# Optimization experiments

Hardware: AMD Instinct MI355X
Metric: run time of the kernel (lower is better)

## Reference

```python
import jax, jax.numpy as jnp
import numpy as np

PATCH = 14

def _patchify(t, p):
    # (B,C,H,W) -> (B*pH*pW, C, p*p)
    B, C, H, W = t.shape
    pH, pW = H // p, W // p
    t = t.reshape(B, C, pH, p, pW, p).transpose(0, 2, 4, 1, 3, 5)
    return t.reshape(B * pH * pW, C, p * p)

def _unpatchify(t, B, C, H, W, p):
    pH, pW = H // p, W // p
    t = t.reshape(B, pH, pW, C, p, p).transpose(0, 3, 1, 4, 2, 5)
    return t.reshape(B, C, H, W)

def setup_inputs() -> dict:
    key = jax.random.key(0)
    ks = jax.random.split(key, 9)
    B, C, H, W = 4, 256, 224, 224
    s = 1.0 / np.sqrt(C)
    return {
        "x": jax.random.normal(ks[0], (B, C, H, W), jnp.float32),
        "skip0": jax.random.normal(ks[1], (B, C, 112, 112), jnp.float32),
        "skip1": jax.random.normal(ks[2], (B, C, 56, 56), jnp.float32),
        "Wq": jax.random.normal(ks[3], (C, C), jnp.float32) * s,
        "bq": jax.random.normal(ks[4], (C,), jnp.float32) * 0.01,
        "Wk": jax.random.normal(ks[5], (C, C), jnp.float32) * s,
        "bk": jax.random.normal(ks[6], (C,), jnp.float32) * 0.01,
        "Wv": jax.random.normal(ks[7], (C, C), jnp.float32) * s,
        "bv": jax.random.normal(ks[8], (C,), jnp.float32) * 0.01,
    }

def reference(x, skip0, skip1, Wq, bq, Wk, bk, Wv, bv):
    B, C, H, W = x.shape
    p = PATCH
    xp = _patchify(x, p)                       # (N, C, L), L = p*p
    # 1x1 conv on x (query) is shared across skips
    Q = jnp.einsum('oc,ncl->nol', Wq, xp) + bq[None, :, None]
    out = 0.0
    for skip in (skip0, skip1):
        sk = jax.image.resize(skip, (B, C, H, W), method='bilinear')  # align_corners=False
        sp = _patchify(sk, p)
        K = jnp.einsum('oc,ncl->nol', Wk, sp) + bk[None, :, None]
        V = jnp.einsum('oc,ncl->nol', Wv, sp) + bv[None, :, None]
        attn = jax.nn.softmax(jnp.einsum('ncl,ncm->nlm', Q, K), axis=-1)  # unscaled, per original
        out = out + jnp.einsum('nlm,ncm->ncl', attn, V)
    return _unpatchify(out, B, C, H, W, p)
```

## Files before the change

### kernel.cpp

```cpp
#include <hip/hip_runtime.h>

typedef _Float16 f16;
typedef _Float16 f16x8 __attribute__((ext_vector_type(8)));
typedef float f32x4 __attribute__((ext_vector_type(4)));

#define DEV static __device__ __forceinline__

constexpr int  NPATCH = 1024;
constexpr int  LLEN   = 196;
constexpr long NLROWS = (long)NPATCH * LLEN;

DEV void g2l16(const void* g, void* l) {
  __builtin_amdgcn_global_load_lds(
      (const __attribute__((address_space(1))) unsigned int*)g,
      (__attribute__((address_space(3))) unsigned int*)l, 16, 0, 0);
}

DEV unsigned pk2(float a, float b) {
  union { f16 h[2]; unsigned u; } z;
  z.h[0] = (f16)a; z.h[1] = (f16)b;
  return z.u;
}

__global__ __launch_bounds__(256) void k0_prep(
    const float* __restrict__ Wq, const float* __restrict__ Wk,
    const float* __restrict__ Wv, const float* __restrict__ bq,
    f16* __restrict__ G16, f16* __restrict__ Wv16, float* __restrict__ u32) {
  int bx = blockIdx.x, t = threadIdx.x;
  if (bx < 256) {
    int c = bx;
    float acc = 0.f;
    for (int o = 0; o < 256; ++o) acc += Wq[o*256 + c] * Wk[o*256 + t];
    G16[c*256 + t] = (f16)acc;
  } else if (bx == 256) {
    float acc = 0.f;
    for (int o = 0; o < 256; ++o) acc += bq[o] * Wk[o*256 + t];
    u32[t] = acc;
  } else {
    for (int r = 0; r < 256; ++r) Wv16[r*256 + t] = (f16)Wv[r*256 + t];
  }
}

__global__ __launch_bounds__(256) void k1_pack(
    const float* __restrict__ src, int Hs, int Ws, float invS,
    f16* __restrict__ dst, float* __restrict__ ub4,
    const float* __restrict__ u32, int do_ub) {
  __shared__ unsigned tile[32 * 225];
  __shared__ float us[64];
  int bx = blockIdx.x;
  int cc0 = (bx & 3) * 64;
  int bi = bx >> 2;
  int i  = bi % 14; bi /= 14;
  int py = bi & 15; int b = bi >> 4;
  int y = py*14 + i;
  int t = threadIdx.x;
  if (t < 64) us[t] = u32[cc0 + t];

  if (invS == 1.0f) {
    int xh = t & 7, pr = t >> 3;
    const float* b0 = src + ((long)(b*256 + cc0 + 2*pr)) * 50176 + y*224;
    const float* b1 = b0 + 50176;
#pragma unroll
    for (int it = 0; it < 7; ++it) {
      int x0 = (it*8 + xh) * 4;
      float4 va = *(const float4*)(b0 + x0);
      float4 vb = *(const float4*)(b1 + x0);
      tile[pr*225 + x0 + 0] = pk2(va.x, vb.x);
      tile[pr*225 + x0 + 1] = pk2(va.y, vb.y);
      tile[pr*225 + x0 + 2] = pk2(va.z, vb.z);
      tile[pr*225 + x0 + 3] = pk2(va.w, vb.w);
    }
  } else {
    float fy  = (y + 0.5f) * invS - 0.5f;
    float y0f = floorf(fy);
    float wy1 = fy - y0f, wy0 = 1.f - wy1;
    int y0 = (int)y0f, y1 = (int)y0f + 1;
    y0 = min(max(y0, 0), Hs-1); y1 = min(max(y1, 0), Hs-1);
    long plane = (long)Hs * Ws;
    int xl = t & 63, c4 = t >> 6;
    for (int xp = 0; xp < 4; ++xp) {
      int x = xp*64 + xl;
      if (x < 224) {
        float fx  = (x + 0.5f) * invS - 0.5f;
        float x0f = floorf(fx);
        float wx1 = fx - x0f, wx0 = 1.f - wx1;
        int x0 = (int)x0f, x1 = (int)x0f + 1;
        x0 = min(max(x0, 0), Ws-1); x1 = min(max(x1, 0), Ws-1);
        int o00 = y0*Ws + x0, o01 = y0*Ws + x1;
        int o10 = y1*Ws + x0, o11 = y1*Ws + x1;
#pragma unroll
        for (int pp = 0; pp < 8; ++pp) {
          int pr = c4*8 + pp;
          const float* base0 = src + ((long)(b*256 + cc0 + 2*pr)) * plane;
          const float* base1 = base0 + plane;
          float va = wy0*(wx0*base0[o00] + wx1*base0[o01])
                   + wy1*(wx0*base0[o10] + wx1*base0[o11]);
          float vb = wy0*(wx0*base1[o00] + wx1*base1[o01])
                   + wy1*(wx0*base1[o10] + wx1*base1[o11]);
          tile[pr*225 + x] = pk2(va, vb);
        }
      }
    }
  }
  __syncthreads();
  int q = t & 7, xg = t >> 3;
  float4 u0, u1;
  if (do_ub) {
    u0 = *(const float4*)(us + q*8);
    u1 = *(const float4*)(us + q*8 + 4);
  }
  for (int xo = 0; xo < 7; ++xo) {
    int x = xo*32 + xg;
    unsigned p0 = tile[(q*4+0)*225 + x];
    unsigned p1 = tile[(q*4+1)*225 + x];
    unsigned p2 = tile[(q*4+2)*225 + x];
    unsigned p3 = tile[(q*4+3)*225 + x];
    int px = x / 14, j = x % 14;
    int m = i*14 + j;
    long nm = (long)(b*256 + py*16 + px) * 196 + m;
    uint4 w; w.x = p0; w.y = p1; w.z = p2; w.w = p3;
    *reinterpret_cast<uint4*>(dst + nm*256 + cc0 + q*8) = w;
    if (do_ub) {
      union { unsigned u; f16 h[2]; } c0, c1, c2, c3;
      c0.u = p0; c1.u = p1; c2.u = p2; c3.u = p3;
      float part = u0.x*(float)c0.h[0] + u0.y*(float)c0.h[1]
                 + u0.z*(float)c1.h[0] + u0.w*(float)c1.h[1]
                 + u1.x*(float)c2.h[0] + u1.y*(float)c2.h[1]
                 + u1.z*(float)c3.h[0] + u1.w*(float)c3.h[1];
      part += __shfl_xor(part, 1);
      part += __shfl_xor(part, 2);
      part += __shfl_xor(part, 4);
      if (q == 0) ub4[(long)(bx & 3) * NLROWS + nm] = part;
    }
  }
}

__global__ __launch_bounds__(256) void k2_kv(
    const f16* __restrict__ SPT, const f16* __restrict__ G16,
    const f16* __restrict__ Wv16, f16* __restrict__ KtT, f16* __restrict__ VT2) {
  __shared__ __align__(16) char ldsA[64 * 80];
  __shared__ __align__(16) char ldsB[512 * 80];
  int tid = threadIdx.x;
  int lane = tid & 63, wv = tid >> 6;
  long nm0 = (long)blockIdx.x * 64;
  f32x4 zero = {0.f, 0.f, 0.f, 0.f};
  f32x4 acc[4][8];
#pragma unroll
  for (int a = 0; a < 4; ++a)
#pragma unroll
    for (int bb = 0; bb < 8; ++bb) acc[a][bb] = zero;
  int col0 = wv * 128;
  int r15 = lane & 15, quad = lane >> 4;
  for (int k0 = 0; k0 < 256; k0 += 32) {
    __syncthreads();
#pragma unroll
    for (int call = 0; call < 2; ++call) {
      int slot = call*256 + tid;
      if (slot < 320) {
        int row = slot / 5, part = slot % 5;
        int pp_ = part < 4 ? part : 0;
        g2l16(SPT + ((nm0 + row)*256 + k0 + pp_*8), ldsA + slot*16);
      }
    }
#pragma unroll
    for (int call = 0; call < 10; ++call) {
      int slot = call*256 + tid;
      int row = slot / 5, part = slot % 5;
      int pp_ = part < 4 ? part : 0;
      const f16* g = (row < 256) ? (G16 + (row*256 + k0 + pp_*8))
                                 : (Wv16 + ((row - 256)*256 + k0 + pp_*8));
      g2l16(g, ldsB + slot*16);
    }
    __syncthreads();
    f16x8 af[4];
#pragma unroll
    for (int rt = 0; rt < 4; ++rt)
      af[rt] = *(const f16x8*)(ldsA + (rt*16 + r15)*80 + quad*16);
#pragma unroll
    for (int tc = 0; tc < 8; ++tc) {
      f16x8 bf = *(const f16x8*)(ldsB + (col0 + tc*16 + r15)*80 + quad*16);
#pragma unroll
      for (int rt = 0; rt < 4; ++rt)
        acc[rt][tc] = __builtin_amdgcn_mfma_f32_16x16x32_f16(af[rt], bf, acc[rt][tc], 0, 0, 0);
    }
  }
  __syncthreads();
  f16* ldsV = (f16*)ldsB;
  if (wv >= 2) {
#pragma unroll
    for (int rt = 0; rt < 4; ++rt)
#pragma unroll
      for (int tc = 0; tc < 8; ++tc) {
        int o = col0 - 256 + tc*16 + r15;
#pragma unroll
        for (int reg = 0; reg < 4; ++reg) {
          int row = rt*16 + quad*4 + reg;
          ldsV[row*258 + o] = (f16)acc[rt][tc][reg];
        }
      }
  } else {
#pragma unroll
    for (int rt = 0; rt < 4; ++rt)
#pragma unroll
      for (int tc = 0; tc < 8; ++tc) {
        int colc = col0 + tc*16 + r15;
#pragma unroll
        for (int reg = 0; reg < 4; ++reg) {
          long row = nm0 + rt*16 + quad*4 + reg;
          KtT[row*256 + colc] = (f16)acc[rt][tc][reg];
        }
      }
  }
  __syncthreads();
  {
    int row = tid & 63;
    long nm = nm0 + row;
    int n = (int)(nm / 196), m = (int)(nm % 196);
    long vbase = ((long)n * 256) * 224 + m;
    int o0 = (tid >> 6) * 64;
    for (int it = 0; it < 64; ++it) {
      int o = o0 + it;
      VT2[vbase + (long)o * 224] = ldsV[row*258 + o];
    }
  }
}

__global__ __launch_bounds__(256) void k3_sv(
    const f16* __restrict__ XT, const f16* __restrict__ KtT,
    const float* __restrict__ ub, const f16* __restrict__ VT2,
    f16* __restrict__ Obuf, int mode) {
  __shared__ __align__(16) char lds[50176];
  __shared__ float ubs[208];
  char* ldsA = lds;
  char* ldsB = lds + 5120;
  char* ldsV = lds + 29696;
  int tid = threadIdx.x;
  int lane = tid & 63, wv = tid >> 6;
  int bx = blockIdx.x;
  int n  = ((bx >> 5) << 3) | (bx & 7);
  int l0 = ((bx >> 3) & 3) * 64;
  long base = (long)n * 196;
  for (int s = tid; s < 208; s += 256) {
    float v = 0.f;
    if (s < 196) {
      long o = base + s;
      v = ub[o] + ub[NLROWS + o] + ub[2*NLROWS + o] + ub[3*NLROWS + o];
    }
    ubs[s] = v;
  }
  f32x4 zero = {0.f, 0.f, 0.f, 0.f};
  f32x4 acc[13];
#pragma unroll
  for (int t = 0; t < 13; ++t) acc[t] = zero;
  int r15 = lane & 15, quad = lane >> 4;
  long vrow = ((long)(n*256)) * 224;

  for (int k0 = 0; k0 < 256; k0 += 32) {
    __syncthreads();
#pragma unroll
    for (int call = 0; call < 2; ++call) {
      int slot = call*256 + tid;
      if (slot < 320) {
        int row = slot / 5, part = slot % 5;
        int pp_ = part < 4 ? part : 0;
        int l = l0 + row; l = l > 195 ? 195 : l;
        g2l16(XT + ((base + l)*256 + k0 + pp_*8), ldsA + slot*16);
      }
    }
#pragma unroll
    for (int call = 0; call < 5; ++call) {
      int slot = call*256 + tid;
      if (slot < 1040) {
        int row = slot / 5, part = slot % 5;
        int pp_ = part < 8 ? (part < 4 ? part : 0) : 0;
        int m = row > 195 ? 195 : row;
        g2l16(KtT + ((base + m)*256 + k0 + pp_*8), ldsB + slot*16);
      }
    }
    __syncthreads();
    f16x8 af = *(const f16x8*)(ldsA + (wv*16 + r15)*80 + quad*16);
#pragma unroll
    for (int t = 0; t < 13; ++t) {
      f16x8 bf = *(const f16x8*)(ldsB + (t*16 + r15)*80 + quad*16);
      acc[t] = __builtin_amdgcn_mfma_f32_16x16x32_f16(af, bf, acc[t], 0, 0, 0);
    }
  }

#pragma unroll
  for (int call = 0; call < 5; ++call) {
    int slot = call*256 + tid;
    int row = slot / 5, part = slot % 5;
    int pp_ = part < 4 ? part : 0;
    g2l16(VT2 + (vrow + (long)row*224 + pp_*8), ldsV + slot*16);
  }

  float mx[4] = {-1e30f, -1e30f, -1e30f, -1e30f};
#pragma unroll
  for (int t = 0; t < 13; ++t) {
    int colb = t*16 + r15;
    float ubv = ubs[colb];
    bool valid = colb < 196;
#pragma unroll
    for (int reg = 0; reg < 4; ++reg) {
      float v = acc[t][reg] + ubv;
      acc[t][reg] = v;
      if (valid) mx[reg] = fmaxf(mx[reg], v);
    }
  }
#pragma unroll
  for (int reg = 0; reg < 4; ++reg) {
    float m = mx[reg];
    m = fmaxf(m, __shfl_xor(m, 1));
    m = fmaxf(m, __shfl_xor(m, 2));
    m = fmaxf(m, __shfl_xor(m, 4));
    m = fmaxf(m, __shfl_xor(m, 8));
    mx[reg] = m;
  }
  float sum[4] = {0.f, 0.f, 0.f, 0.f};
#pragma unroll
  for (int t = 0; t < 13; ++t) {
    int colb = t*16 + r15;
    bool valid = colb < 196;
#pragma unroll
    for (int reg = 0; reg < 4; ++reg) {
      float p = valid ? __expf(acc[t][reg] - mx[reg]) : 0.f;
      acc[t][reg] = p;
      sum[reg] += p;
    }
  }
#pragma unroll
  for (int reg = 0; reg < 4; ++reg) {
    float s = sum[reg];
    s += __shfl_xor(s, 1);
    s += __shfl_xor(s, 2);
    s += __shfl_xor(s, 4);
    s += __shfl_xor(s, 8);
    sum[reg] = 1.0f / s;
  }

  __syncthreads();
#pragma unroll
  for (int reg = 0; reg < 4; ++reg) {
    int row = wv*16 + quad*4 + reg;
    float sc = sum[reg];
#pragma unroll
    for (int t = 0; t < 13; ++t)
      *(f16*)(lds + row*464 + (t*16 + r15)*2) = (f16)(acc[t][reg] * sc);
  }
  {
    int row = tid >> 2, mq = tid & 3;
    *(long*)(lds + row*464 + 416 + mq*8) = 0;
  }

  f32x4 oacc[16];
#pragma unroll
  for (int t = 0; t < 16; ++t) oacc[t] = zero;
  for (int it = 0; it < 7; ++it) {
    if (it > 0) {
      __syncthreads();
#pragma unroll
      for (int call = 0; call < 5; ++call) {
        int slot = call*256 + tid;
        int row = slot / 5, part = slot % 5;
        int pp_ = part < 4 ? part : 0;
        g2l16(VT2 + (vrow + (long)row*224 + it*32 + pp_*8), ldsV + slot*16);
      }
    }
    __syncthreads();
    f16x8 af = *(const f16x8*)(lds + (wv*16 + r15)*464 + it*64 + quad*16);
#pragma unroll
    for (int t = 0; t < 16; ++t) {
      f16x8 bf = *(const f16x8*)(ldsV + (t*16 + r15)*80 + quad*16);
      oacc[t] = __builtin_amdgcn_mfma_f32_16x16x32_f16(af, bf, oacc[t], 0, 0, 0);
    }
  }

#pragma unroll
  for (int reg = 0; reg < 4; ++reg) {
    int l = l0 + wv*16 + quad*4 + reg;
    if (l < 196) {
      long orow = (base + l) * 256;
#pragma unroll
      for (int t = 0; t < 16; ++t) {
        int c = t*16 + r15;
        float v = oacc[t][reg];
        if (mode == 0) Obuf[orow + c] = (f16)v;
        else           Obuf[orow + c] = (f16)(v + (float)Obuf[orow + c]);
      }
    }
  }
}

__global__ __launch_bounds__(256) void k5_unpatch(
    const f16* __restrict__ Obuf, const float* __restrict__ bv,
    float* __restrict__ out) {
  __shared__ float lds[64 * 225];
  int bx = blockIdx.x;
  int cc = (bx & 3) * 64;  bx >>= 2;
  int i  = bx % 14; bx /= 14;
  int py = bx & 15; int b = bx >> 4;
  int t = threadIdx.x;
  int cl = t & 63, pg = t >> 6;
  for (int it = 0; it < 56; ++it) {
    int pr = it*4 + pg;
    int px = pr / 14, j = pr % 14;
    int n = b*256 + py*16 + px;
    float v = (float)Obuf[((long)n*196 + i*14 + j)*256 + cc + cl];
    lds[cl*225 + px*14 + j] = v;
  }
  __syncthreads();
  int yy = py*14 + i;
  for (int c = 0; c < 64; ++c) {
    float bb = 2.0f * bv[cc + c];
    if (t < 224)
      out[(((long)(b*256 + cc + c))*224 + yy)*224 + t] = lds[c*225 + t] + bb;
  }
}

extern "C" void kernel_launch(void* const* d_in, const int* in_sizes, int n_in,
                              void* d_out, int out_size, void* d_ws, size_t ws_size,
                              hipStream_t stream) {
  (void)in_sizes; (void)n_in; (void)out_size; (void)ws_size;
  const float* x     = (const float*)d_in[0];
  const float* skip0 = (const float*)d_in[1];
  const float* skip1 = (const float*)d_in[2];
  const float* Wq    = (const float*)d_in[3];
  const float* bq    = (const float*)d_in[4];
  const float* Wk    = (const float*)d_in[5];
  const float* Wv    = (const float*)d_in[7];
  const float* bv    = (const float*)d_in[8];
  float* out = (float*)d_out;

  char* ws = (char*)d_ws;
  size_t off = 0;
  auto alloc = [&](size_t bytes) {
    char* p = ws + off;
    off += (bytes + 255) & ~(size_t)255;
    return p;
  };
  f16*   XT   = (f16*)  alloc((size_t)NLROWS * 256 * 2);
  f16*   SPT  = (f16*)  alloc((size_t)NLROWS * 256 * 2);
  f16*   KtT  = (f16*)  alloc((size_t)NLROWS * 256 * 2);
  f16*   VT2  = (f16*)  alloc((size_t)NPATCH * 256 * 224 * 2);
  f16*   Obuf = (f16*)  alloc((size_t)NLROWS * 256 * 2);
  float* ub   = (float*)alloc((size_t)NLROWS * 4 * 4);
  f16*   G16  = (f16*)  alloc(256 * 256 * 2);
  f16*   Wv16 = (f16*)  alloc(256 * 256 * 2);
  float* u32  = (float*)alloc(256 * 4);

  k0_prep<<<258, 256, 0, stream>>>(Wq, Wk, Wv, bq, G16, Wv16, u32);
  k1_pack<<<3584, 256, 0, stream>>>(x, 224, 224, 1.0f, XT, nullptr, u32, 0);

  const float* skips[2] = {skip0, skip1};
  int   hs[2]   = {112, 56};
  float invs[2] = {0.5f, 0.25f};
  for (int s = 0; s < 2; ++s) {
    k1_pack<<<3584, 256, 0, stream>>>(skips[s], hs[s], hs[s], invs[s], SPT, ub, u32, 1);
    k2_kv<<<3136, 256, 0, stream>>>(SPT, G16, Wv16, KtT, VT2);
    k3_sv<<<4096, 256, 0, stream>>>(XT, KtT, ub, VT2, Obuf, s);
  }
  k5_unpatch<<<3584, 256, 0, stream>>>(Obuf, bv, out);
}
```

Baseline: 1.556 ms.

## Load K and V operands directly from global memory in the attention kernel

Restructures k3_sv so the 64x256 query tile is staged once into an XOR-swizzled LDS buffer and kept in registers. The K^T and V operands are now read straight from global memory into MFMA registers instead of being staged through LDS with per-step barriers. LDS use shrinks and most __syncthreads disappear, which should raise occupancy and cut synchronisation. The cost is that each wave issues redundant global loads for K and V, relying on L1/L2 to absorb them, and the register count rises.

```diff
diff --git a/kernel.cpp b/kernel.cpp
--- a/kernel.cpp
+++ b/kernel.cpp
@@ -229,17 +229,16 @@
     const f16* __restrict__ XT, const f16* __restrict__ KtT,
     const float* __restrict__ ub, const f16* __restrict__ VT2,
     f16* __restrict__ Obuf, int mode) {
-  __shared__ __align__(16) char lds[50176];
+  __shared__ __align__(16) char lds[64 * 512];
   __shared__ float ubs[208];
-  char* ldsA = lds;
-  char* ldsB = lds + 5120;
-  char* ldsV = lds + 29696;
   int tid = threadIdx.x;
   int lane = tid & 63, wv = tid >> 6;
   int bx = blockIdx.x;
   int n  = ((bx >> 5) << 3) | (bx & 7);
   int l0 = ((bx >> 3) & 3) * 64;
   long base = (long)n * 196;
+  int r15 = lane & 15, quad = lane >> 4;
+
   for (int s = tid; s < 208; s += 256) {
     float v = 0.f;
     if (s < 196) {
@@ -248,50 +247,36 @@
     }
     ubs[s] = v;
   }
+
+#pragma unroll
+  for (int call = 0; call < 8; ++call) {
+    int slot = call*256 + tid;
+    int row = slot >> 5, sc = slot & 31;
+    int l = l0 + row; l = l > 195 ? 195 : l;
+    int gc = sc ^ (row & 7);
+    g2l16(XT + ((base + l)*256 + gc*8), lds + slot*16);
+  }
+  __syncthreads();
+
+  int arow = wv*16 + r15;
+  f16x8 af[8];
+#pragma unroll
+  for (int ks = 0; ks < 8; ++ks)
+    af[ks] = *(const f16x8*)(lds + arow*512 + (((ks*4 + quad) ^ (arow & 7)) * 16));
+
   f32x4 zero = {0.f, 0.f, 0.f, 0.f};
   f32x4 acc[13];
 #pragma unroll
   for (int t = 0; t < 13; ++t) acc[t] = zero;
-  int r15 = lane & 15, quad = lane >> 4;
-  long vrow = ((long)(n*256)) * 224;
-
-  for (int k0 = 0; k0 < 256; k0 += 32) {
-    __syncthreads();
-#pragma unroll
-    for (int call = 0; call < 2; ++call) {
-      int slot = call*256 + tid;
-      if (slot < 320) {
-        int row = slot / 5, part = slot % 5;
-        int pp_ = part < 4 ? part : 0;
-        int l = l0 + row; l = l > 195 ? 195 : l;
-        g2l16(XT + ((base + l)*256 + k0 + pp_*8), ldsA + slot*16);
-      }
-    }
-#pragma unroll
-    for (int call = 0; call < 5; ++call) {
-      int slot = call*256 + tid;
-      if (slot < 1040) {
-        int row = slot / 5, part = slot % 5;
-        int pp_ = part < 8 ? (part < 4 ? part : 0) : 0;
-        int m = row > 195 ? 195 : row;
-        g2l16(KtT + ((base + m)*256 + k0 + pp_*8), ldsB + slot*16);
-      }
-    }
-    __syncthreads();
-    f16x8 af = *(const f16x8*)(ldsA + (wv*16 + r15)*80 + quad*16);
-#pragma unroll
-    for (int t = 0; t < 13; ++t) {
-      f16x8 bf = *(const f16x8*)(ldsB + (t*16 + r15)*80 + quad*16);
-      acc[t] = __builtin_amdgcn_mfma_f32_16x16x32_f16(af, bf, acc[t], 0, 0, 0);
-    }
-  }
-
-#pragma unroll
-  for (int call = 0; call < 5; ++call) {
-    int slot = call*256 + tid;
-    int row = slot / 5, part = slot % 5;
-    int pp_ = part < 4 ? part : 0;
-    g2l16(VT2 + (vrow + (long)row*224 + pp_*8), ldsV + slot*16);
+#pragma unroll
+  for (int t = 0; t < 13; ++t) {
+    int m = t*16 + r15; m = m > 195 ? 195 : m;
+    const f16* kp = KtT + (base + m)*256 + quad*8;
+#pragma unroll
+    for (int ks = 0; ks < 8; ++ks) {
+      f16x8 bf = *(const f16x8*)(kp + ks*32);
+      acc[t] = __builtin_amdgcn_mfma_f32_16x16x32_f16(af[ks], bf, acc[t], 0, 0, 0);
+    }
   }
 
   float mx[4] = {-1e30f, -1e30f, -1e30f, -1e30f};
@@ -351,39 +336,30 @@
     int row = tid >> 2, mq = tid & 3;
     *(long*)(lds + row*464 + 416 + mq*8) = 0;
   }
-
-  f32x4 oacc[16];
-#pragma unroll
-  for (int t = 0; t < 16; ++t) oacc[t] = zero;
-  for (int it = 0; it < 7; ++it) {
-    if (it > 0) {
-      __syncthreads();
-#pragma unroll
-      for (int call = 0; call < 5; ++call) {
-        int slot = call*256 + tid;
-        int row = slot / 5, part = slot % 5;
-        int pp_ = part < 4 ? part : 0;
-        g2l16(VT2 + (vrow + (long)row*224 + it*32 + pp_*8), ldsV + slot*16);
-      }
-    }
-    __syncthreads();
-    f16x8 af = *(const f16x8*)(lds + (wv*16 + r15)*464 + it*64 + quad*16);
-#pragma unroll
-    for (int t = 0; t < 16; ++t) {
-      f16x8 bf = *(const f16x8*)(ldsV + (t*16 + r15)*80 + quad*16);
-      oacc[t] = __builtin_amdgcn_mfma_f32_16x16x32_f16(af, bf, oacc[t], 0, 0, 0);
-    }
-  }
-
-#pragma unroll
-  for (int reg = 0; reg < 4; ++reg) {
-    int l = l0 + wv*16 + quad*4 + reg;
-    if (l < 196) {
-      long orow = (base + l) * 256;
-#pragma unroll
-      for (int t = 0; t < 16; ++t) {
-        int c = t*16 + r15;
-        float v = oacc[t][reg];
+  __syncthreads();
+
+  f16x8 pa[7];
+#pragma unroll
+  for (int it = 0; it < 7; ++it)
+    pa[it] = *(const f16x8*)(lds + (wv*16 + r15)*464 + it*64 + quad*16);
+
+  long vrow = ((long)(n*256)) * 224;
+#pragma unroll
+  for (int t = 0; t < 16; ++t) {
+    const f16* vpt = VT2 + vrow + (long)(t*16 + r15)*224 + quad*8;
+    f32x4 o = zero;
+#pragma unroll
+    for (int it = 0; it < 7; ++it) {
+      f16x8 bf = *(const f16x8*)(vpt + it*32);
+      o = __builtin_amdgcn_mfma_f32_16x16x32_f16(pa[it], bf, o, 0, 0, 0);
+    }
+    int c = t*16 + r15;
+#pragma unroll
+    for (int reg = 0; reg < 4; ++reg) {
+      int l = l0 + wv*16 + quad*4 + reg;
+      if (l < 196) {
+        long orow = (base + l) * 256;
+        float v = o[reg];
         if (mode == 0) Obuf[orow + c] = (f16)v;
         else           Obuf[orow + c] = (f16)(v + (float)Obuf[orow + c]);
       }
```

Result: slower. 2.003 ms (+28.7%).

## Keep Q fragments in registers and widen K-chunk staging in score kernel

Applied to the files above, without the earlier changes.

The score GEMM in k3_sv now loads each wave's Q (XT) fragments straight from global memory into registers once, instead of staging them through LDS every k-step. The K tile is staged in 64-wide chunks (4 iterations instead of 8), which halves the number of barrier pairs. In the PV GEMM, all seven probability fragments are read from LDS into registers up front rather than once per iteration. The register arrays are indexed by loop variables, so if the compiler does not fully unroll those loops it may spill them to scratch, and register pressure rises, which can lower occupancy.

```diff
diff --git a/kernel.cpp b/kernel.cpp
--- a/kernel.cpp
+++ b/kernel.cpp
@@ -229,17 +229,25 @@
     const f16* __restrict__ XT, const f16* __restrict__ KtT,
     const float* __restrict__ ub, const f16* __restrict__ VT2,
     f16* __restrict__ Obuf, int mode) {
-  __shared__ __align__(16) char lds[50176];
+  __shared__ __align__(16) char lds[50432];
   __shared__ float ubs[208];
-  char* ldsA = lds;
-  char* ldsB = lds + 5120;
-  char* ldsV = lds + 29696;
+  char* ldsB = lds;
+  char* ldsV = lds + 29952;
   int tid = threadIdx.x;
   int lane = tid & 63, wv = tid >> 6;
   int bx = blockIdx.x;
   int n  = ((bx >> 5) << 3) | (bx & 7);
   int l0 = ((bx >> 3) & 3) * 64;
   long base = (long)n * 196;
+  int r15 = lane & 15, quad = lane >> 4;
+
+  int al = l0 + wv*16 + r15; al = al > 195 ? 195 : al;
+  const f16* ap = XT + (base + al)*256 + quad*8;
+  f16x8 af[8];
+#pragma unroll
+  for (int ks = 0; ks < 8; ++ks)
+    af[ks] = *(const f16x8*)(ap + ks*32);
+
   for (int s = tid; s < 208; s += 256) {
     float v = 0.f;
     if (s < 196) {
@@ -248,44 +256,37 @@
     }
     ubs[s] = v;
   }
+
   f32x4 zero = {0.f, 0.f, 0.f, 0.f};
   f32x4 acc[13];
 #pragma unroll
   for (int t = 0; t < 13; ++t) acc[t] = zero;
-  int r15 = lane & 15, quad = lane >> 4;
+
+  for (int kc = 0; kc < 4; ++kc) {
+    __syncthreads();
+#pragma unroll
+    for (int call = 0; call < 8; ++call) {
+      int slot = call*256 + tid;
+      if (slot < 1872) {
+        int row = slot / 9, part = slot % 9;
+        int pp_ = part < 8 ? part : 0;
+        int m = row > 195 ? 195 : row;
+        g2l16(KtT + ((base + m)*256 + kc*64 + pp_*8), ldsB + slot*16);
+      }
+    }
+    __syncthreads();
+#pragma unroll
+    for (int ks = 0; ks < 2; ++ks) {
+      f16x8 a = af[kc*2 + ks];
+#pragma unroll
+      for (int t = 0; t < 13; ++t) {
+        f16x8 bf = *(const f16x8*)(ldsB + (t*16 + r15)*144 + (ks*4 + quad)*16);
+        acc[t] = __builtin_amdgcn_mfma_f32_16x16x32_f16(a, bf, acc[t], 0, 0, 0);
+      }
+    }
+  }
+
   long vrow = ((long)(n*256)) * 224;
-
-  for (int k0 = 0; k0 < 256; k0 += 32) {
-    __syncthreads();
-#pragma unroll
-    for (int call = 0; call < 2; ++call) {
-      int slot = call*256 + tid;
-      if (slot < 320) {
-        int row = slot / 5, part = slot % 5;
-        int pp_ = part < 4 ? part : 0;
-        int l = l0 + row; l = l > 195 ? 195 : l;
-        g2l16(XT + ((base + l)*256 + k0 + pp_*8), ldsA + slot*16);
-      }
-    }
-#pragma unroll
-    for (int call = 0; call < 5; ++call) {
-      int slot = call*256 + tid;
-      if (slot < 1040) {
-        int row = slot / 5, part = slot % 5;
-        int pp_ = part < 8 ? (part < 4 ? part : 0) : 0;
-        int m = row > 195 ? 195 : row;
-        g2l16(KtT + ((base + m)*256 + k0 + pp_*8), ldsB + slot*16);
-      }
-    }
-    __syncthreads();
-    f16x8 af = *(const f16x8*)(ldsA + (wv*16 + r15)*80 + quad*16);
-#pragma unroll
-    for (int t = 0; t < 13; ++t) {
-      f16x8 bf = *(const f16x8*)(ldsB + (t*16 + r15)*80 + quad*16);
-      acc[t] = __builtin_amdgcn_mfma_f32_16x16x32_f16(af, bf, acc[t], 0, 0, 0);
-    }
-  }
-
 #pragma unroll
   for (int call = 0; call < 5; ++call) {
     int slot = call*256 + tid;
@@ -355,6 +356,7 @@
   f32x4 oacc[16];
 #pragma unroll
   for (int t = 0; t < 16; ++t) oacc[t] = zero;
+  f16x8 pa[7];
   for (int it = 0; it < 7; ++it) {
     if (it > 0) {
       __syncthreads();
@@ -367,11 +369,16 @@
       }
     }
     __syncthreads();
-    f16x8 af = *(const f16x8*)(lds + (wv*16 + r15)*464 + it*64 + quad*16);
+    if (it == 0) {
+#pragma unroll
+      for (int j = 0; j < 7; ++j)
+        pa[j] = *(const f16x8*)(lds + (wv*16 + r15)*464 + j*64 + quad*16);
+    }
+    f16x8 a = pa[it];
 #pragma unroll
     for (int t = 0; t < 16; ++t) {
       f16x8 bf = *(const f16x8*)(ldsV + (t*16 + r15)*80 + quad*16);
-      oacc[t] = __builtin_amdgcn_mfma_f32_16x16x32_f16(af, bf, oacc[t], 0, 0, 0);
+      oacc[t] = __builtin_amdgcn_mfma_f32_16x16x32_f16(a, bf, oacc[t], 0, 0, 0);
     }
   }
 
```

After: 1.960 ms. 1.26x slower.
